# Optimization experiments

Measured on AMD Instinct MI355X. Metric: run time of the kernel, lower is better.

The kernel has to match this reference:

```python
import jax, jax.numpy as jnp
import numpy as np


def setup_inputs() -> dict:
    key = jax.random.key(0)
    kx, ky = jax.random.split(key)
    B, Sx, Sy, D = 8, 2048, 2048, 128
    x = jax.random.normal(kx, (B, Sx, D), dtype=jnp.float32)
    y = jax.random.normal(ky, (B, Sy, D), dtype=jnp.float32)
    return {"x": x, "y": y}


def reference(x, y):
    # score[b, i, j] = softmax_j(x[b,i,:] . y[b,j,:])
    score = jax.nn.softmax(jnp.einsum("bid,bjd->bij", x, y), axis=-1)
    # dropout is identity in eval mode (reference baseline)
    att_map = jnp.einsum("bij,bjd->bid", score, y)
    return x + att_map
```

## Files before the change

kernel.cpp:

```cpp
#include <hip/hip_runtime.h>
#include <hip/hip_fp16.h>


#define SX 2048
#define SY 2048
#define DD 128
#define KVBLK 64
#define NWAVE 8
#define QBLK (NWAVE * 32)
#define NTHREADS (NWAVE * 64)
#define L2E 1.4426950408889634f

typedef __attribute__((ext_vector_type(8))) _Float16 f16x8;
typedef __attribute__((ext_vector_type(4))) _Float16 f16x4;
typedef __attribute__((ext_vector_type(4))) float f32x4;
typedef __attribute__((ext_vector_type(16))) float f32x16;
typedef __attribute__((ext_vector_type(4))) unsigned int u32x4;

__global__ __launch_bounds__(256) void prepass(const float* __restrict__ y,
                                               _Float16* __restrict__ yT)
{
    __shared__ _Float16 T[64 * 64];
    char* Tb = (char*)T;
    const int tid = (int)threadIdx.x;
    const int b = blockIdx.y;
    const int k0 = (blockIdx.x >> 1) * 64;
    const int d0 = (blockIdx.x & 1) * 64;
    const float* yb = y + (size_t)b * SY * DD;
#pragma unroll
    for (int t = 0; t < 2; ++t) {
        int cid = t * 256 + tid;
        int row = cid >> 3, c = cid & 7;
        const float* gp = yb + (size_t)(k0 + row) * DD + d0 + c * 8;
        f32x4 a0 = *(const f32x4*)gp;
        f32x4 a1 = *(const f32x4*)(gp + 4);
        f16x8 v;
#pragma unroll
        for (int j = 0; j < 4; ++j) { v[j] = (_Float16)a0[j]; v[4 + j] = (_Float16)a1[j]; }
        *(f16x8*)(Tb + ((row * 128 + c * 16) ^ ((row & 7) << 4))) = v;
    }
    __syncthreads();
#pragma unroll
    for (int t = 0; t < 2; ++t) {
        int cid = t * 256 + tid;
        int drow = cid >> 3, ck = cid & 7;
        f16x8 v;
#pragma unroll
        for (int j = 0; j < 8; ++j)
            v[j] = *(const _Float16*)(Tb + ((((ck * 8 + j) * 128) + drow * 2) ^ (j << 4)));
        *(f16x8*)(yT + ((size_t)b * DD + d0 + drow) * SY + k0 + ck * 8) = v;
    }
}

template<bool SPLITOUT, bool USEYT>
__global__ __launch_bounds__(NTHREADS) void attn_fwd(
    const float* __restrict__ xg, const float* __restrict__ yg,
    const _Float16* __restrict__ yT,
    float* __restrict__ og, _Float16* __restrict__ Opart,
    float* __restrict__ mpart, float* __restrict__ lpart,
    int kv_len, int nb)
{
    __shared__ __align__(16) unsigned char smem[32768];
    char* Kb = (char*)smem;
    char* Vb = (char*)smem + 16384;

    const int tid = (int)threadIdx.x;
    const int lane = tid & 63;
    const int wv = tid >> 6;
    const int l31 = lane & 31;
    const int hi = lane >> 5;
    const int swz = (l31 & 7) << 4;
    const int b = blockIdx.y;
    const int qbase = blockIdx.x * QBLK;
    const int sp = blockIdx.z;
    const int kv_begin = sp * kv_len;
    const int ntiles = kv_len / KVBLK;

    const float* xb = xg + (size_t)b * SX * DD;
    const float* yb = yg + (size_t)b * SY * DD;

    const int qrow = qbase + wv * 32 + l31;
    f16x8 qreg[8];
#pragma unroll
    for (int kst = 0; kst < 8; ++kst) {
        const float* qp = xb + (size_t)qrow * DD + kst * 16 + hi * 8;
        f32x4 q0 = *(const f32x4*)qp;
        f32x4 q1 = *(const f32x4*)(qp + 4);
        f16x8 v;
#pragma unroll
        for (int j = 0; j < 4; ++j) { v[j] = (_Float16)q0[j]; v[4 + j] = (_Float16)q1[j]; }
        qreg[kst] = v;
    }

    f32x4 ks[4];
    f16x8 vs[2];

    auto LOADT = [&](int kv0) {
#pragma unroll
        for (int c = 0; c < 2; ++c) {
            int cid = c * NTHREADS + tid;
            int krow = cid >> 4, kc8 = cid & 15;
            const float* gp = yb + (size_t)(kv0 + krow) * DD + kc8 * 8;
            ks[c * 2]     = *(const f32x4*)gp;
            ks[c * 2 + 1] = *(const f32x4*)(gp + 4);
        }
        if constexpr (USEYT) {
#pragma unroll
            for (int c = 0; c < 2; ++c) {
                int cid = c * NTHREADS + tid;
                int d = cid >> 3, kc = cid & 7;
                vs[c] = *(const f16x8*)(yT + ((size_t)b * DD + d) * SY + kv0 + kc * 8);
            }
        }
    };
    auto STORET = [&]() {
#pragma unroll
        for (int c = 0; c < 2; ++c) {
            int cid = c * NTHREADS + tid;
            int krow = cid >> 4, kc8 = cid & 15;
            f16x8 kv;
#pragma unroll
            for (int j = 0; j < 4; ++j) { kv[j] = (_Float16)ks[c * 2][j]; kv[4 + j] = (_Float16)ks[c * 2 + 1][j]; }
            *(f16x8*)(Kb + ((krow * 256 + kc8 * 16) ^ ((krow & 7) << 4))) = kv;
            if constexpr (!USEYT) {
#pragma unroll
                for (int j = 0; j < 8; ++j) {
                    int d = kc8 * 8 + j;
                    *(_Float16*)(Vb + ((d * 128 + krow * 2) ^ ((d & 7) << 4))) = kv[j];
                }
            }
        }
        if constexpr (USEYT) {
#pragma unroll
            for (int c = 0; c < 2; ++c) {
                int cid = c * NTHREADS + tid;
                int d = cid >> 3, kc = cid & 7;
                *(f16x8*)(Vb + ((d * 128 + kc * 16) ^ ((d & 7) << 4))) = vs[c];
            }
        }
    };

    f32x16 o[4];
#pragma unroll
    for (int dt = 0; dt < 4; ++dt) o[dt] = f32x16{};
    float m = -3.0e38f, ls = 0.f;

    LOADT(kv_begin);
    for (int t = 0; t < ntiles; ++t) {
        __syncthreads();
        STORET();
        if (t + 1 < ntiles) LOADT(kv_begin + (t + 1) * KVBLK);
        __syncthreads();

        f32x16 sc[2];
        __builtin_amdgcn_s_setprio(1);
#pragma unroll
        for (int s = 0; s < 2; ++s) {
            f32x16 acc = f32x16{};
#pragma unroll
            for (int kst = 0; kst < 8; ++kst) {
                f16x8 kf = *(const f16x8*)(Kb + (((32 * s + l31) * 256 + kst * 32 + hi * 16) ^ swz));
                acc = __builtin_amdgcn_mfma_f32_32x32x16_f16(kf, qreg[kst], acc, 0, 0, 0);
            }
            sc[s] = acc;
        }
        __builtin_amdgcn_s_setprio(0);

        float tv[16];
#pragma unroll
        for (int r = 0; r < 16; ++r) tv[r] = fmaxf(sc[0][r], sc[1][r]);
#pragma unroll
        for (int st = 8; st >= 1; st >>= 1)
#pragma unroll
            for (int i = 0; i < 8; ++i)
                if (i < st) tv[i] = fmaxf(tv[i], tv[i + st]);
        float tm = tv[0];
        tm = fmaxf(tm, __shfl_xor(tm, 32, 64));
        float mn = fmaxf(m, tm);
        float al = __builtin_exp2f((m - mn) * L2E);
        float mnl = mn * L2E;
        m = mn;
        float sv[16];
#pragma unroll
        for (int r = 0; r < 16; ++r) {
            float p0 = __builtin_exp2f(__builtin_fmaf(sc[0][r], L2E, -mnl));
            float p1 = __builtin_exp2f(__builtin_fmaf(sc[1][r], L2E, -mnl));
            sc[0][r] = p0; sc[1][r] = p1;
            sv[r] = p0 + p1;
        }
#pragma unroll
        for (int st = 8; st >= 1; st >>= 1)
#pragma unroll
            for (int i = 0; i < 8; ++i)
                if (i < st) sv[i] += sv[i + st];
        float ps = sv[0];
        ps += __shfl_xor(ps, 32, 64);
        ls = ls * al + ps;
#pragma unroll
        for (int dt = 0; dt < 4; ++dt)
#pragma unroll
            for (int r = 0; r < 16; ++r) o[dt][r] *= al;

#pragma unroll
        for (int s = 0; s < 2; ++s) {
#pragma unroll
            for (int k = 0; k < 2; ++k) {
                unsigned aw = __builtin_bit_cast(unsigned, __builtin_amdgcn_cvt_pkrtz(sc[s][8 * k + 0], sc[s][8 * k + 1]));
                unsigned cw = __builtin_bit_cast(unsigned, __builtin_amdgcn_cvt_pkrtz(sc[s][8 * k + 2], sc[s][8 * k + 3]));
                unsigned bw = __builtin_bit_cast(unsigned, __builtin_amdgcn_cvt_pkrtz(sc[s][8 * k + 4], sc[s][8 * k + 5]));
                unsigned dw = __builtin_bit_cast(unsigned, __builtin_amdgcn_cvt_pkrtz(sc[s][8 * k + 6], sc[s][8 * k + 7]));
                unsigned pa = __shfl_xor(aw, 32, 64);
                unsigned pb = __shfl_xor(bw, 32, 64);
                unsigned pc = __shfl_xor(cw, 32, 64);
                unsigned pd = __shfl_xor(dw, 32, 64);
                u32x4 ww;
                ww[0] = hi ? pb : aw;
                ww[1] = hi ? pd : cw;
                ww[2] = hi ? bw : pa;
                ww[3] = hi ? dw : pc;
                f16x8 pf = __builtin_bit_cast(f16x8, ww);
                __builtin_amdgcn_s_setprio(1);
#pragma unroll
                for (int dt = 0; dt < 4; ++dt) {
                    f16x8 vf = *(const f16x8*)(Vb + (((dt * 32 + l31) * 128 + 64 * s + 32 * k + 16 * hi) ^ swz));
                    o[dt] = __builtin_amdgcn_mfma_f32_32x32x16_f16(vf, pf, o[dt], 0, 0, 0);
                }
                __builtin_amdgcn_s_setprio(0);
            }
        }
    }

    float inv = SPLITOUT ? 1.0f : (1.0f / ls);
    if constexpr (SPLITOUT) {
        if (lane < 32) {
            size_t mi = ((size_t)sp * nb + b) * SX + qrow;
            mpart[mi] = m;
            lpart[mi] = ls;
        }
    }
    __syncthreads();
    char* Ep = (char*)smem + wv * 4096;
    for (int dt = 0; dt < 4; ++dt) {
#pragma unroll
        for (int g = 0; g < 4; ++g)
#pragma unroll
            for (int t4 = 0; t4 < 4; ++t4) {
                int r = g * 4 + t4;
                int dl = t4 + 8 * g + 4 * hi;
                *(float*)(Ep + (l31 * 128 + ((dl * 4) ^ swz))) = o[dt][r] * inv;
            }
        __syncthreads();
        if constexpr (SPLITOUT) {
            _Float16* Ob = Opart + ((size_t)sp * nb + b) * SX * DD;
#pragma unroll
            for (int i = 0; i < 2; ++i) {
                int id = i * 64 + lane;
                int q2 = id >> 2, c8 = id & 3;
                int qs = (q2 & 7) << 4;
                f32x4 e0 = *(const f32x4*)(Ep + (q2 * 128 + ((c8 * 32) ^ qs)));
                f32x4 e1 = *(const f32x4*)(Ep + (q2 * 128 + ((c8 * 32 + 16) ^ qs)));
                f16x8 h;
#pragma unroll
                for (int j = 0; j < 4; ++j) { h[j] = (_Float16)e0[j]; h[4 + j] = (_Float16)e1[j]; }
                *(f16x8*)(Ob + (size_t)(qbase + wv * 32 + q2) * DD + dt * 32 + c8 * 8) = h;
            }
        } else {
            float* ob = og + (size_t)b * SX * DD;
#pragma unroll
            for (int i = 0; i < 4; ++i) {
                int id = i * 64 + lane;
                int q2 = id >> 3, ch = id & 7;
                int qs = (q2 & 7) << 4;
                f32x4 e = *(const f32x4*)(Ep + (q2 * 128 + ((ch * 16) ^ qs)));
                size_t gi = (size_t)(qbase + wv * 32 + q2) * DD + dt * 32 + ch * 4;
                f32x4 xv = *(const f32x4*)(xb + gi);
                f32x4 rs;
#pragma unroll
                for (int j = 0; j < 4; ++j) rs[j] = xv[j] + e[j];
                *(f32x4*)(ob + gi) = rs;
            }
        }
        __syncthreads();
    }
}

__global__ __launch_bounds__(256) void combine(const float* __restrict__ x,
    const _Float16* __restrict__ Opart, const float* __restrict__ mpart,
    const float* __restrict__ lpart, float* __restrict__ out, int nb, int nsplit)
{
    int tid = (int)threadIdx.x;
    int gr = blockIdx.x * 8 + (tid >> 5);
    int c = tid & 31;
    size_t nrows = (size_t)nb * SX;
    float M = -3.0e38f;
    for (int s = 0; s < nsplit; ++s) M = fmaxf(M, mpart[(size_t)s * nrows + gr]);
    float wsum = 0.f;
    float acc[4] = {0.f, 0.f, 0.f, 0.f};
    for (int s = 0; s < nsplit; ++s) {
        float ms = mpart[(size_t)s * nrows + gr];
        float lv = lpart[(size_t)s * nrows + gr];
        float wv = __builtin_exp2f((ms - M) * L2E);
        wsum += wv * lv;
        f16x4 h = *(const f16x4*)(Opart + (size_t)s * nrows * DD + (size_t)gr * DD + c * 4);
#pragma unroll
        for (int j = 0; j < 4; ++j) acc[j] += wv * (float)h[j];
    }
    float inv = 1.0f / wsum;
    size_t off = (size_t)gr * DD + c * 4;
    f32x4 xv = *(const f32x4*)(x + off);
    f32x4 rs;
#pragma unroll
    for (int j = 0; j < 4; ++j) rs[j] = xv[j] + acc[j] * inv;
    *(f32x4*)(out + off) = rs;
}

extern "C" void kernel_launch(void* const* d_in, const int* in_sizes, int n_in,
                              void* d_out, int out_size, void* d_ws, size_t ws_size,
                              hipStream_t stream) {
    const float* x = (const float*)d_in[0];
    const float* y = (const float*)d_in[1];
    float* out = (float*)d_out;
    int nb = in_sizes[0] / (SX * DD);

    size_t yTsz = (size_t)nb * DD * SY * sizeof(_Float16);
    auto opsz = [&](int n) { return (size_t)n * nb * SX * DD * sizeof(_Float16); };
    auto mlsz = [&](int n) { return (size_t)n * nb * SX * sizeof(float); };
    char* w = (char*)d_ws;
    _Float16* yT = (_Float16*)w;
    bool haveYT = yTsz <= ws_size;

    int nsplit = 0;
    if (haveYT) {
        if (yTsz + opsz(4) + 2 * mlsz(4) <= ws_size) nsplit = 4;
        else if (yTsz + opsz(2) + 2 * mlsz(2) <= ws_size) nsplit = 2;
    }

    if (haveYT)
        prepass<<<dim3((SY / 64) * (DD / 64), nb), 256, 0, stream>>>(y, yT);

    if (nsplit >= 2) {
        _Float16* Op = (_Float16*)(w + yTsz);
        float* mp = (float*)(w + yTsz + opsz(nsplit));
        float* lp = mp + (size_t)nsplit * nb * SX;
        attn_fwd<true, true><<<dim3(SX / QBLK, nb, nsplit), NTHREADS, 0, stream>>>(
            x, y, yT, out, Op, mp, lp, SY / nsplit, nb);
        combine<<<dim3(nb * SX / 8), 256, 0, stream>>>(x, Op, mp, lp, out, nb, nsplit);
    } else if (haveYT) {
        attn_fwd<false, true><<<dim3(SX / QBLK, nb, 1), NTHREADS, 0, stream>>>(
            x, y, yT, out, nullptr, nullptr, nullptr, SY, nb);
    } else {
        attn_fwd<false, false><<<dim3(SX / QBLK, nb, 1), NTHREADS, 0, stream>>>(
            x, y, nullptr, out, nullptr, nullptr, nullptr, SY, nb);
    }
}
```

Baseline: 51.37 us.

## Double-buffer KV tiles, prestage fp16 K, lazy softmax rescale, 4-wave blocks

The prepass now also writes an fp16 row-major copy of y, so the attention kernel loads K as half precision instead of converting fp32 each tile. K/V tiles are double-buffered in LDS with a two-ahead register prefetch, leaving one barrier per tile. Block size drops to 4 waves, and the online-softmax rescale is skipped unless the running max grows by more than a threshold, as in FA4-style lazy rescaling. The epilogue swaps barriers for per-wave lgkmcnt waits. This costs extra workspace and prepass writes, doubles LDS per block, and relies on the threshold keeping fp16 P values in range.

```diff
diff --git a/kernel.cpp b/kernel.cpp
--- a/kernel.cpp
+++ b/kernel.cpp
@@ -6,10 +6,11 @@
 #define SY 2048
 #define DD 128
 #define KVBLK 64
-#define NWAVE 8
+#define NWAVE 4
 #define QBLK (NWAVE * 32)
 #define NTHREADS (NWAVE * 64)
 #define L2E 1.4426950408889634f
+#define RTHR 8.0f
 
 typedef __attribute__((ext_vector_type(8))) _Float16 f16x8;
 typedef __attribute__((ext_vector_type(4))) _Float16 f16x4;
@@ -17,7 +18,9 @@
 typedef __attribute__((ext_vector_type(16))) float f32x16;
 typedef __attribute__((ext_vector_type(4))) unsigned int u32x4;
 
+template<bool WRITEB>
 __global__ __launch_bounds__(256) void prepass(const float* __restrict__ y,
+                                               _Float16* __restrict__ yB,
                                                _Float16* __restrict__ yT)
 {
     __shared__ _Float16 T[64 * 64];
@@ -37,6 +40,8 @@
         f16x8 v;
 #pragma unroll
         for (int j = 0; j < 4; ++j) { v[j] = (_Float16)a0[j]; v[4 + j] = (_Float16)a1[j]; }
+        if constexpr (WRITEB)
+            *(f16x8*)(yB + ((size_t)b * SY + k0 + row) * DD + d0 + c * 8) = v;
         *(f16x8*)(Tb + ((row * 128 + c * 16) ^ ((row & 7) << 4))) = v;
     }
     __syncthreads();
@@ -52,17 +57,15 @@
     }
 }
 
-template<bool SPLITOUT, bool USEYT>
+template<bool SPLITOUT, int MODE>
 __global__ __launch_bounds__(NTHREADS) void attn_fwd(
     const float* __restrict__ xg, const float* __restrict__ yg,
-    const _Float16* __restrict__ yT,
+    const _Float16* __restrict__ yB, const _Float16* __restrict__ yT,
     float* __restrict__ og, _Float16* __restrict__ Opart,
     float* __restrict__ mpart, float* __restrict__ lpart,
     int kv_len, int nb)
 {
-    __shared__ __align__(16) unsigned char smem[32768];
-    char* Kb = (char*)smem;
-    char* Vb = (char*)smem + 16384;
+    __shared__ __align__(16) unsigned char smem[2][32768];
 
     const int tid = (int)threadIdx.x;
     const int lane = tid & 63;
@@ -74,7 +77,7 @@
     const int qbase = blockIdx.x * QBLK;
     const int sp = blockIdx.z;
     const int kv_begin = sp * kv_len;
-    const int ntiles = kv_len / KVBLK;
+    const int nt = kv_len / KVBLK;
 
     const float* xb = xg + (size_t)b * SX * DD;
     const float* yb = yg + (size_t)b * SY * DD;
@@ -92,37 +95,46 @@
         qreg[kst] = v;
     }
 
-    f32x4 ks[4];
-    f16x8 vs[2];
+    f16x8 kh[4];
+    f32x4 kf[8];
+    f16x8 vh[4];
 
     auto LOADT = [&](int kv0) {
 #pragma unroll
-        for (int c = 0; c < 2; ++c) {
+        for (int c = 0; c < 4; ++c) {
             int cid = c * NTHREADS + tid;
             int krow = cid >> 4, kc8 = cid & 15;
-            const float* gp = yb + (size_t)(kv0 + krow) * DD + kc8 * 8;
-            ks[c * 2]     = *(const f32x4*)gp;
-            ks[c * 2 + 1] = *(const f32x4*)(gp + 4);
-        }
-        if constexpr (USEYT) {
-#pragma unroll
-            for (int c = 0; c < 2; ++c) {
+            if constexpr (MODE == 2) {
+                kh[c] = *(const f16x8*)(yB + ((size_t)b * SY + kv0 + krow) * DD + kc8 * 8);
+            } else {
+                const float* gp = yb + (size_t)(kv0 + krow) * DD + kc8 * 8;
+                kf[c * 2]     = *(const f32x4*)gp;
+                kf[c * 2 + 1] = *(const f32x4*)(gp + 4);
+            }
+        }
+        if constexpr (MODE >= 1) {
+#pragma unroll
+            for (int c = 0; c < 4; ++c) {
                 int cid = c * NTHREADS + tid;
                 int d = cid >> 3, kc = cid & 7;
-                vs[c] = *(const f16x8*)(yT + ((size_t)b * DD + d) * SY + kv0 + kc * 8);
+                vh[c] = *(const f16x8*)(yT + ((size_t)b * DD + d) * SY + kv0 + kc * 8);
             }
         }
     };
-    auto STORET = [&]() {
-#pragma unroll
-        for (int c = 0; c < 2; ++c) {
+    auto STORET = [&](char* Kb, char* Vb) {
+#pragma unroll
+        for (int c = 0; c < 4; ++c) {
             int cid = c * NTHREADS + tid;
             int krow = cid >> 4, kc8 = cid & 15;
             f16x8 kv;
-#pragma unroll
-            for (int j = 0; j < 4; ++j) { kv[j] = (_Float16)ks[c * 2][j]; kv[4 + j] = (_Float16)ks[c * 2 + 1][j]; }
+            if constexpr (MODE == 2) {
+                kv = kh[c];
+            } else {
+#pragma unroll
+                for (int j = 0; j < 4; ++j) { kv[j] = (_Float16)kf[c * 2][j]; kv[4 + j] = (_Float16)kf[c * 2 + 1][j]; }
+            }
             *(f16x8*)(Kb + ((krow * 256 + kc8 * 16) ^ ((krow & 7) << 4))) = kv;
-            if constexpr (!USEYT) {
+            if constexpr (MODE == 0) {
 #pragma unroll
                 for (int j = 0; j < 8; ++j) {
                     int d = kc8 * 8 + j;
@@ -130,12 +142,12 @@
                 }
             }
         }
-        if constexpr (USEYT) {
-#pragma unroll
-            for (int c = 0; c < 2; ++c) {
+        if constexpr (MODE >= 1) {
+#pragma unroll
+            for (int c = 0; c < 4; ++c) {
                 int cid = c * NTHREADS + tid;
                 int d = cid >> 3, kc = cid & 7;
-                *(f16x8*)(Vb + ((d * 128 + kc * 16) ^ ((d & 7) << 4))) = vs[c];
+                *(f16x8*)(Vb + ((d * 128 + kc * 16) ^ ((d & 7) << 4))) = vh[c];
             }
         }
     };
@@ -146,11 +158,18 @@
     float m = -3.0e38f, ls = 0.f;
 
     LOADT(kv_begin);
-    for (int t = 0; t < ntiles; ++t) {
-        __syncthreads();
-        STORET();
-        if (t + 1 < ntiles) LOADT(kv_begin + (t + 1) * KVBLK);
-        __syncthreads();
+    STORET((char*)smem[0], (char*)smem[0] + 16384);
+    if (nt > 1) LOADT(kv_begin + KVBLK);
+    __syncthreads();
+
+    for (int t = 0; t < nt; ++t) {
+        char* Kb = (char*)smem[t & 1];
+        char* Vb = Kb + 16384;
+        if (t + 1 < nt) {
+            char* Kn = (char*)smem[(t + 1) & 1];
+            STORET(Kn, Kn + 16384);
+        }
+        if (t + 2 < nt) LOADT(kv_begin + (t + 2) * KVBLK);
 
         f32x16 sc[2];
         __builtin_amdgcn_s_setprio(1);
@@ -159,8 +178,8 @@
             f32x16 acc = f32x16{};
 #pragma unroll
             for (int kst = 0; kst < 8; ++kst) {
-                f16x8 kf = *(const f16x8*)(Kb + (((32 * s + l31) * 256 + kst * 32 + hi * 16) ^ swz));
-                acc = __builtin_amdgcn_mfma_f32_32x32x16_f16(kf, qreg[kst], acc, 0, 0, 0);
+                f16x8 kfr = *(const f16x8*)(Kb + (((32 * s + l31) * 256 + kst * 32 + hi * 16) ^ swz));
+                acc = __builtin_amdgcn_mfma_f32_32x32x16_f16(kfr, qreg[kst], acc, 0, 0, 0);
             }
             sc[s] = acc;
         }
@@ -176,10 +195,17 @@
                 if (i < st) tv[i] = fmaxf(tv[i], tv[i + st]);
         float tm = tv[0];
         tm = fmaxf(tm, __shfl_xor(tm, 32, 64));
-        float mn = fmaxf(m, tm);
-        float al = __builtin_exp2f((m - mn) * L2E);
-        float mnl = mn * L2E;
-        m = mn;
+        if (!__all(tm <= m + RTHR)) {
+            float mn = fmaxf(m, tm);
+            float al = __builtin_exp2f((m - mn) * L2E);
+            m = mn;
+            ls *= al;
+#pragma unroll
+            for (int dt = 0; dt < 4; ++dt)
+#pragma unroll
+                for (int r = 0; r < 16; ++r) o[dt][r] *= al;
+        }
+        float mnl = m * L2E;
         float sv[16];
 #pragma unroll
         for (int r = 0; r < 16; ++r) {
@@ -195,11 +221,7 @@
                 if (i < st) sv[i] += sv[i + st];
         float ps = sv[0];
         ps += __shfl_xor(ps, 32, 64);
-        ls = ls * al + ps;
-#pragma unroll
-        for (int dt = 0; dt < 4; ++dt)
-#pragma unroll
-            for (int r = 0; r < 16; ++r) o[dt][r] *= al;
+        ls += ps;
 
 #pragma unroll
         for (int s = 0; s < 2; ++s) {
@@ -228,6 +250,7 @@
                 __builtin_amdgcn_s_setprio(0);
             }
         }
+        __syncthreads();
     }
 
     float inv = SPLITOUT ? 1.0f : (1.0f / ls);
@@ -238,8 +261,7 @@
             lpart[mi] = ls;
         }
     }
-    __syncthreads();
-    char* Ep = (char*)smem + wv * 4096;
+    char* Ep = (char*)smem[0] + wv * 4096;
     for (int dt = 0; dt < 4; ++dt) {
 #pragma unroll
         for (int g = 0; g < 4; ++g)
@@ -249,7 +271,7 @@
                 int dl = t4 + 8 * g + 4 * hi;
                 *(float*)(Ep + (l31 * 128 + ((dl * 4) ^ swz))) = o[dt][r] * inv;
             }
-        __syncthreads();
+        asm volatile("s_waitcnt lgkmcnt(0)" ::: "memory");
         if constexpr (SPLITOUT) {
             _Float16* Ob = Opart + ((size_t)sp * nb + b) * SX * DD;
 #pragma unroll
@@ -280,7 +302,7 @@
                 *(f32x4*)(ob + gi) = rs;
             }
         }
-        __syncthreads();
+        asm volatile("s_waitcnt lgkmcnt(0)" ::: "memory");
     }
 }
 
@@ -322,34 +344,48 @@
     float* out = (float*)d_out;
     int nb = in_sizes[0] / (SX * DD);
 
-    size_t yTsz = (size_t)nb * DD * SY * sizeof(_Float16);
+    size_t yBsz = (size_t)nb * SY * DD * sizeof(_Float16);
+    size_t yTsz = yBsz;
     auto opsz = [&](int n) { return (size_t)n * nb * SX * DD * sizeof(_Float16); };
     auto mlsz = [&](int n) { return (size_t)n * nb * SX * sizeof(float); };
     char* w = (char*)d_ws;
-    _Float16* yT = (_Float16*)w;
-    bool haveYT = yTsz <= ws_size;
-
-    int nsplit = 0;
-    if (haveYT) {
-        if (yTsz + opsz(4) + 2 * mlsz(4) <= ws_size) nsplit = 4;
-        else if (yTsz + opsz(2) + 2 * mlsz(2) <= ws_size) nsplit = 2;
-    }
-
-    if (haveYT)
-        prepass<<<dim3((SY / 64) * (DD / 64), nb), 256, 0, stream>>>(y, yT);
-
-    if (nsplit >= 2) {
+    dim3 pgrid((SY / 64) * (DD / 64), nb);
+
+    if (ws_size >= yBsz + yTsz + opsz(4) + 2 * mlsz(4)) {
+        _Float16* yB = (_Float16*)w;
+        _Float16* yT = (_Float16*)(w + yBsz);
+        _Float16* Op = (_Float16*)(w + yBsz + yTsz);
+        float* mp = (float*)(w + yBsz + yTsz + opsz(4));
+        float* lp = mp + (size_t)4 * nb * SX;
+        prepass<true><<<pgrid, 256, 0, stream>>>(y, yB, yT);
+        attn_fwd<true, 2><<<dim3(SX / QBLK, nb, 4), NTHREADS, 0, stream>>>(
+            x, y, yB, yT, out, Op, mp, lp, SY / 4, nb);
+        combine<<<dim3(nb * SX / 8), 256, 0, stream>>>(x, Op, mp, lp, out, nb, 4);
+    } else if (ws_size >= yTsz + opsz(4) + 2 * mlsz(4)) {
+        _Float16* yT = (_Float16*)w;
         _Float16* Op = (_Float16*)(w + yTsz);
-        float* mp = (float*)(w + yTsz + opsz(nsplit));
-        float* lp = mp + (size_t)nsplit * nb * SX;
-        attn_fwd<true, true><<<dim3(SX / QBLK, nb, nsplit), NTHREADS, 0, stream>>>(
-            x, y, yT, out, Op, mp, lp, SY / nsplit, nb);
-        combine<<<dim3(nb * SX / 8), 256, 0, stream>>>(x, Op, mp, lp, out, nb, nsplit);
-    } else if (haveYT) {
-        attn_fwd<false, true><<<dim3(SX / QBLK, nb, 1), NTHREADS, 0, stream>>>(
-            x, y, yT, out, nullptr, nullptr, nullptr, SY, nb);
+        float* mp = (float*)(w + yTsz + opsz(4));
+        float* lp = mp + (size_t)4 * nb * SX;
+        prepass<false><<<pgrid, 256, 0, stream>>>(y, nullptr, yT);
+        attn_fwd<true, 1><<<dim3(SX / QBLK, nb, 4), NTHREADS, 0, stream>>>(
+            x, y, nullptr, yT, out, Op, mp, lp, SY / 4, nb);
+        combine<<<dim3(nb * SX / 8), 256, 0, stream>>>(x, Op, mp, lp, out, nb, 4);
+    } else if (ws_size >= yTsz + opsz(2) + 2 * mlsz(2)) {
+        _Float16* yT = (_Float16*)w;
+        _Float16* Op = (_Float16*)(w + yTsz);
+        float* mp = (float*)(w + yTsz + opsz(2));
+        float* lp = mp + (size_t)2 * nb * SX;
+        prepass<false><<<pgrid, 256, 0, stream>>>(y, nullptr, yT);
+        attn_fwd<true, 1><<<dim3(SX / QBLK, nb, 2), NTHREADS, 0, stream>>>(
+            x, y, nullptr, yT, out, Op, mp, lp, SY / 2, nb);
+        combine<<<dim3(nb * SX / 8), 256, 0, stream>>>(x, Op, mp, lp, out, nb, 2);
+    } else if (ws_size >= yTsz) {
+        _Float16* yT = (_Float16*)w;
+        prepass<false><<<pgrid, 256, 0, stream>>>(y, nullptr, yT);
+        attn_fwd<false, 1><<<dim3(SX / QBLK, nb, 1), NTHREADS, 0, stream>>>(
+            x, y, nullptr, yT, out, nullptr, nullptr, nullptr, SY, nb);
     } else {
-        attn_fwd<false, false><<<dim3(SX / QBLK, nb, 1), NTHREADS, 0, stream>>>(
-            x, y, nullptr, out, nullptr, nullptr, nullptr, SY, nb);
+        attn_fwd<false, 0><<<dim3(SX / QBLK, nb, 1), NTHREADS, 0, stream>>>(
+            x, y, nullptr, nullptr, out, nullptr, nullptr, nullptr, SY, nb);
     }
 }
```

Result: slower. 64.23 us (+25.0%).
